# Kernel optimization log

Hardware: AMD Instinct MI355X
Metric: run time of the kernel (lower is better)

## Reference

```python
import jax, jax.numpy as jnp
import numpy as np

EPS_MIN = 1e-8
N_ITER = 50  # solver_iter


def solve_qp_simplex(M, n_iter=N_ITER):
    """Frank-Wolfe min over the simplex of alpha^T M alpha. M: (B,K,K) -> alpha: (B,K)."""
    B, K, _ = M.shape
    alpha0 = jnp.full((B, K), 1.0 / K, dtype=M.dtype)

    def step(alpha, it):
        grad = 2.0 * jnp.einsum('bij,bj->bi', M, alpha)           # (B,K)
        idx = jnp.argmin(grad, axis=1)                             # (B,)
        s = jax.nn.one_hot(idx, K, dtype=alpha.dtype)              # vertex of simplex
        gamma = 2.0 / (it + 2.0)
        return (1.0 - gamma) * alpha + gamma * s, None

    alpha, _ = jax.lax.scan(step, alpha0, jnp.arange(n_iter, dtype=M.dtype))
    return alpha


def _raw_loss(scores, targets, C):
    B, K = scores.shape
    # epsilon = offdiag_mean of C per batch, scaled by 1.0, clamped
    offdiag_mean = (C.sum(axis=(1, 2)) - jnp.trace(C, axis1=1, axis2=2)) / (K * K - K)
    eps = jnp.maximum(offdiag_mean, EPS_MIN)                       # (B,)

    f = 0.5 * scores
    exponent = -(f[:, :, None] + f[:, None, :] + C) / eps[:, None, None]  # (B,K,K)
    shift = exponent.max(axis=(1, 2), keepdims=True)
    logM = exponent - shift
    M = jnp.exp(logM)

    # solver is an implicit layer: non-differentiable by construction
    alpha = jax.lax.stop_gradient(solve_qp_simplex(M, N_ITER))     # (B,K)

    pos = alpha > 0
    loga = jnp.where(pos, jnp.log(jnp.where(pos, alpha, 1.0)), -jnp.inf)
    term = loga[:, :, None] + loga[:, None, :] + logM              # (B,K,K)
    logval = jax.scipy.special.logsumexp(term.reshape(B, K * K), axis=1)
    conjugate = -eps * (logval + shift.reshape(B))

    f_y = jnp.take_along_axis(scores, targets[:, None], axis=1)[:, 0]
    return conjugate - f_y


def setup_inputs() -> dict:
    key = jax.random.key(0)
    k1, k2, k3 = jax.random.split(key, 3)
    B, K = 512, 256
    scores = jax.random.normal(k1, (B, K), dtype=jnp.float32)
    targets = jax.random.randint(k2, (B,), 0, K)
    C = jax.random.uniform(k3, (B, K, K), dtype=jnp.float32)
    return {"scores": scores, "targets": targets, "C": C}


def reference(scores, targets, C):
    return _raw_loss(scores, targets, C).mean()
```

## Files before the change

### kernel.cpp

```cpp
#include <hip/hip_runtime.h>
#include <math.h>

#define KDIM 256
#define NITER 50


__global__ __launch_bounds__(256) void k1_partials(
    const float* __restrict__ scores, const float* __restrict__ C,
    float* __restrict__ psum_o, float* __restrict__ ptrace_o, float* __restrict__ pmin_o)
{
    const int blk = blockIdx.x;
    const int b = blk >> 2, chunk = blk & 3;
    const int tid = threadIdx.x, lane = tid & 63, wave = tid >> 6;
    const float4* C4 = (const float4*)(C + (size_t)b * KDIM * KDIM);

    __shared__ float4 sf4[KDIM/4];
    __shared__ float redS[256], redT[256], redM[256];
    const float* sf = (const float*)sf4;
    ((float*)sf4)[tid] = 0.5f * scores[b*KDIM + tid];
    __syncthreads();

    const int row0 = chunk * 64;
    float psum = 0.f, ptrace = 0.f, pmin = INFINITY;
    #pragma unroll
    for (int rr = 0; rr < 16; ++rr) {
        const int row = row0 + wave + rr*4;
        float4 c4 = C4[row*(KDIM/4) + lane];
        float frow = sf[row];
        float4 fj = sf4[lane];
        psum += (c4.x + c4.y) + (c4.z + c4.w);
        pmin = fminf(pmin, fminf(fminf(frow+fj.x+c4.x, frow+fj.y+c4.y),
                                 fminf(frow+fj.z+c4.z, frow+fj.w+c4.w)));
        if ((row >> 2) == lane) {
            int r2 = row & 3;
            ptrace += (r2==0) ? c4.x : (r2==1) ? c4.y : (r2==2) ? c4.z : c4.w;
        }
    }
    redS[tid] = psum; redT[tid] = ptrace; redM[tid] = pmin;
    __syncthreads();
    for (int s = 128; s > 0; s >>= 1) {
        if (tid < s) {
            redS[tid] += redS[tid+s];
            redT[tid] += redT[tid+s];
            redM[tid]  = fminf(redM[tid], redM[tid+s]);
        }
        __syncthreads();
    }
    if (tid == 0) { psum_o[blk] = redS[0]; ptrace_o[blk] = redT[0]; pmin_o[blk] = redM[0]; }
}

__global__ __launch_bounds__(512) void k23_fw(
    const float* __restrict__ scores, const int* __restrict__ targets,
    const float* __restrict__ C,
    const float* __restrict__ psum_i, const float* __restrict__ ptrace_i, const float* __restrict__ pmin_i,
    float* __restrict__ lossB)
{
    const int b = blockIdx.x;
    const int tid = threadIdx.x, lane = tid & 63, wave = tid >> 6;
    const float* Cb = C + (size_t)b * KDIM * KDIM;
    const float4* C4 = (const float4*)Cb;

    __shared__ float4 sf4[KDIM/4];
    __shared__ float rs[KDIM];
    __shared__ float aAll[KDIM];
    __shared__ int   wcnt[8];
    __shared__ int   sIdx[64];
    __shared__ float sLog[64];
    __shared__ float wm[8], wsm[8];

    const float* sf = (const float*)sf4;
    if (tid < KDIM) ((float*)sf4)[tid] = 0.5f * scores[b*KDIM + tid];
    __syncthreads();

    float sum = 0.f, tr = 0.f, mn = INFINITY;
    #pragma unroll
    for (int c2 = 0; c2 < 4; ++c2) {
        sum += psum_i[b*4 + c2];
        tr  += ptrace_i[b*4 + c2];
        mn   = fminf(mn, pmin_i[b*4 + c2]);
    }
    const float eps = fmaxf((sum - tr) / (float)(KDIM*KDIM - KDIM), 1e-8f);
    const float inv_eps = 1.0f / eps;
    const float minv = mn;

    #pragma unroll 8
    for (int rr = 0; rr < 32; ++rr) {
        const int row = rr*8 + wave;
        float4 c4 = C4[row*(KDIM/4) + lane];
        float frow = sf[row];
        float4 fj = sf4[lane];
        float p = __expf((minv - (frow+fj.x+c4.x)) * inv_eps)
                + __expf((minv - (frow+fj.y+c4.y)) * inv_eps)
                + __expf((minv - (frow+fj.z+c4.z)) * inv_eps)
                + __expf((minv - (frow+fj.w+c4.w)) * inv_eps);
        #pragma unroll
        for (int off = 32; off > 0; off >>= 1) p += __shfl_xor(p, off);
        if (lane == 0) rs[row] = p;
    }
    __syncthreads();

    if (wave == 0) {
        const float f0 = sf[lane], f1 = sf[lane+64], f2 = sf[lane+128], f3 = sf[lane+192];
        const float* r0 = Cb + (size_t)lane*KDIM;
        const float* r1 = r0 + 64*KDIM;
        const float* r2 = r0 + 128*KDIM;
        const float* r3 = r0 + 192*KDIM;

        float v = rs[lane]; int vi = lane;
        float t;
        t = rs[lane+64];  if (t < v) { v = t; vi = lane+64; }
        t = rs[lane+128]; if (t < v) { v = t; vi = lane+128; }
        t = rs[lane+192]; if (t < v) { v = t; vi = lane+192; }
        #pragma unroll
        for (int off = 32; off > 0; off >>= 1) {
            float ov = __shfl_xor(v, off);
            int  ovi = __shfl_xor(vi, off);
            if (ov < v || (ov == v && ovi < vi)) { v = ov; vi = ovi; }
        }
        const int idx0 = vi;

        float fidx = sf[idx0];
        float g0 = 2.0f * __expf((minv - (f0 + fidx + r0[idx0])) * inv_eps);
        float g1 = 2.0f * __expf((minv - (f1 + fidx + r1[idx0])) * inv_eps);
        float g2 = 2.0f * __expf((minv - (f2 + fidx + r2[idx0])) * inv_eps);
        float g3 = 2.0f * __expf((minv - (f3 + fidx + r3[idx0])) * inv_eps);
        float a0 = (lane     == idx0) ? 1.0f : 0.0f;
        float a1 = (lane+64  == idx0) ? 1.0f : 0.0f;
        float a2 = (lane+128 == idx0) ? 1.0f : 0.0f;
        float a3 = (lane+192 == idx0) ? 1.0f : 0.0f;

        for (int it = 1; it < NITER; ++it) {
            float v2 = g0; int vi2 = lane;
            if (g1 < v2) { v2 = g1; vi2 = lane+64; }
            if (g2 < v2) { v2 = g2; vi2 = lane+128; }
            if (g3 < v2) { v2 = g3; vi2 = lane+192; }
            #pragma unroll
            for (int off = 32; off > 0; off >>= 1) {
                float ov = __shfl_xor(v2, off);
                int  ovi = __shfl_xor(vi2, off);
                if (ov < v2 || (ov == v2 && ovi < vi2)) { v2 = ov; vi2 = ovi; }
            }
            const int idx = vi2;
            const float gamma = 2.0f / ((float)it + 2.0f);
            const float omg = 1.0f - gamma;
            const int which = idx >> 6;
            float fsel = (which==0) ? f0 : (which==1) ? f1 : (which==2) ? f2 : f3;
            const float fidx2 = __shfl(fsel, idx & 63);
            const float c0 = r0[idx], c1 = r1[idx], c2_ = r2[idx], c3 = r3[idx];
            g0 = omg*g0 + 2.0f*gamma*__expf((minv - (f0 + fidx2 + c0)) * inv_eps);
            g1 = omg*g1 + 2.0f*gamma*__expf((minv - (f1 + fidx2 + c1)) * inv_eps);
            g2 = omg*g2 + 2.0f*gamma*__expf((minv - (f2 + fidx2 + c2_)) * inv_eps);
            g3 = omg*g3 + 2.0f*gamma*__expf((minv - (f3 + fidx2 + c3)) * inv_eps);
            a0 = omg*a0 + ((lane     == idx) ? gamma : 0.0f);
            a1 = omg*a1 + ((lane+64  == idx) ? gamma : 0.0f);
            a2 = omg*a2 + ((lane+128 == idx) ? gamma : 0.0f);
            a3 = omg*a3 + ((lane+192 == idx) ? gamma : 0.0f);
        }
        aAll[lane]     = a0;
        aAll[lane+64]  = a1;
        aAll[lane+128] = a2;
        aAll[lane+192] = a3;
    }
    __syncthreads();

    const float a = (tid < KDIM) ? aAll[tid] : 0.f;

    unsigned long long mask = __ballot(a > 0.f);
    if (lane == 0) wcnt[wave] = __popcll(mask);
    __syncthreads();
    int off0 = 0;
    for (int w = 0; w < wave; ++w) off0 += wcnt[w];
    int count = 0;
    #pragma unroll
    for (int w = 0; w < 8; ++w) count += wcnt[w];
    if (a > 0.f) {
        int pos = off0 + __popcll(mask & ((1ull << lane) - 1ull));
        sIdx[pos] = tid;
        sLog[pos] = logf(a);
    }
    __syncthreads();

    float m = -INFINITY, ss = 0.f;
    const int total = count * count;
    for (int p = tid; p < total; p += 512) {
        int ii = p / count;
        int jj = p - ii * count;
        int i = sIdx[ii], j = sIdx[jj];
        float cij = Cb[i*KDIM + j];
        float lm = (minv - (sf[i] + sf[j] + cij)) * inv_eps;
        float tt = sLog[ii] + sLog[jj] + lm;
        if (tt > m) { ss = ss * __expf(m - tt) + 1.0f; m = tt; }
        else        { ss += __expf(tt - m); }
    }
    #pragma unroll
    for (int off = 32; off > 0; off >>= 1) {
        float om = __shfl_xor(m, off);
        float os = __shfl_xor(ss, off);
        if (os > 0.f) {
            if (ss <= 0.f)   { m = om; ss = os; }
            else if (om > m) { ss = ss*__expf(m-om) + os; m = om; }
            else             { ss += os*__expf(om-m); }
        }
    }
    if (lane == 0) { wm[wave] = m; wsm[wave] = ss; }
    __syncthreads();
    if (tid == 0) {
        float M = wm[0], S = wsm[0];
        #pragma unroll
        for (int w = 1; w < 8; ++w) {
            float om = wm[w], os = wsm[w];
            if (os > 0.f) {
                if (S <= 0.f)    { M = om; S = os; }
                else if (om > M) { S = S*__expf(M-om) + os; M = om; }
                else             { S += os*__expf(om-M); }
            }
        }
        float logval = M + logf(S);
        float shift = -minv * inv_eps;
        float conjugate = -eps * (logval + shift);
        float fy = scores[b*KDIM + targets[b]];
        lossB[b] = conjugate - fy;
    }
}

__global__ __launch_bounds__(512) void cacis_reduce(const float* __restrict__ lossB,
                                                    float* __restrict__ out, int B)
{
    __shared__ float red[512];
    int t = threadIdx.x;
    red[t] = (t < B) ? lossB[t] : 0.f;
    __syncthreads();
    for (int s = 256; s > 0; s >>= 1) { if (t < s) red[t] += red[t+s]; __syncthreads(); }
    if (t == 0) out[0] = red[0] / (float)B;
}

extern "C" void kernel_launch(void* const* d_in, const int* in_sizes, int n_in,
                              void* d_out, int out_size, void* d_ws, size_t ws_size,
                              hipStream_t stream) {
    const float* scores  = (const float*)d_in[0];
    const int*   targets = (const int*)d_in[1];
    const float* C       = (const float*)d_in[2];
    float* out = (float*)d_out;
    const int B = in_sizes[1];

    float* ws     = (float*)d_ws;
    float* psum   = ws;
    float* ptrace = ws + 2048;
    float* pmin   = ws + 4096;
    float* lossB  = ws + 6144;

    k1_partials<<<B*4, 256, 0, stream>>>(scores, C, psum, ptrace, pmin);
    k23_fw     <<<B,   512, 0, stream>>>(scores, targets, C, psum, ptrace, pmin, lossB);
    cacis_reduce<<<1, 512, 0, stream>>>(lossB, out, B);
}
```

Baseline: 107.9 us.

## Fuse stats and Frank-Wolfe kernels, caching C as fp16 in swizzled LDS

Merges the partial-statistics kernel and the Frank-Wolfe kernel into one 1024-thread block per batch row. Each C matrix is read from global memory once and stored in shared memory as fp16 with an XOR swizzle, so the row-sum, solver and logsumexp stages reuse it from LDS instead of re-reading global memory. This removes a kernel launch and the second full pass over C. In exchange, the 128KB LDS footprint limits occupancy to one block per CU, and C loses precision because it is rounded to half.

```diff
diff --git a/kernel.cpp b/kernel.cpp
--- a/kernel.cpp
+++ b/kernel.cpp
@@ -1,98 +1,89 @@
 #include <hip/hip_runtime.h>
+#include <hip/hip_fp16.h>
 #include <math.h>
 
 #define KDIM 256
 #define NITER 50
 
-
-__global__ __launch_bounds__(256) void k1_partials(
-    const float* __restrict__ scores, const float* __restrict__ C,
-    float* __restrict__ psum_o, float* __restrict__ ptrace_o, float* __restrict__ pmin_o)
+__global__ __launch_bounds__(1024, 1) void cacis_one(
+    const float* __restrict__ scores, const int* __restrict__ targets,
+    const float* __restrict__ C, float* __restrict__ lossB)
 {
-    const int blk = blockIdx.x;
-    const int b = blk >> 2, chunk = blk & 3;
+    const int b = blockIdx.x;
     const int tid = threadIdx.x, lane = tid & 63, wave = tid >> 6;
     const float4* C4 = (const float4*)(C + (size_t)b * KDIM * KDIM);
 
-    __shared__ float4 sf4[KDIM/4];
-    __shared__ float redS[256], redT[256], redM[256];
-    const float* sf = (const float*)sf4;
-    ((float*)sf4)[tid] = 0.5f * scores[b*KDIM + tid];
-    __syncthreads();
-
-    const int row0 = chunk * 64;
+    __shared__ __half Ch[KDIM*KDIM];
+    __shared__ float sf[KDIM];
+    __shared__ float rs[KDIM];
+    __shared__ float aAll[KDIM];
+    __shared__ float wS[16], wT[16], wM[16];
+    __shared__ float bc2[2];
+    __shared__ int   wcnt[16];
+    __shared__ int   sIdx[64];
+    __shared__ float sLog[64];
+    __shared__ float wm[16], wsm[16];
+
+    if (tid < KDIM) sf[tid] = 0.5f * scores[b*KDIM + tid];
+    __syncthreads();
+
+    const int c0 = lane * 4;
+    const float fj0 = sf[c0], fj1 = sf[c0+1], fj2 = sf[c0+2], fj3 = sf[c0+3];
+
     float psum = 0.f, ptrace = 0.f, pmin = INFINITY;
     #pragma unroll
     for (int rr = 0; rr < 16; ++rr) {
-        const int row = row0 + wave + rr*4;
+        const int row = rr*16 + wave;
         float4 c4 = C4[row*(KDIM/4) + lane];
-        float frow = sf[row];
-        float4 fj = sf4[lane];
+        const float frow = sf[row];
         psum += (c4.x + c4.y) + (c4.z + c4.w);
-        pmin = fminf(pmin, fminf(fminf(frow+fj.x+c4.x, frow+fj.y+c4.y),
-                                 fminf(frow+fj.z+c4.z, frow+fj.w+c4.w)));
+        pmin = fminf(pmin, fminf(fminf(frow+fj0+c4.x, frow+fj1+c4.y),
+                                 fminf(frow+fj2+c4.z, frow+fj3+c4.w)));
         if ((row >> 2) == lane) {
             int r2 = row & 3;
             ptrace += (r2==0) ? c4.x : (r2==1) ? c4.y : (r2==2) ? c4.z : c4.w;
         }
-    }
-    redS[tid] = psum; redT[tid] = ptrace; redM[tid] = pmin;
-    __syncthreads();
-    for (int s = 128; s > 0; s >>= 1) {
-        if (tid < s) {
-            redS[tid] += redS[tid+s];
-            redT[tid] += redT[tid+s];
-            redM[tid]  = fminf(redM[tid], redM[tid+s]);
-        }
-        __syncthreads();
-    }
-    if (tid == 0) { psum_o[blk] = redS[0]; ptrace_o[blk] = redT[0]; pmin_o[blk] = redM[0]; }
-}
-
-__global__ __launch_bounds__(512) void k23_fw(
-    const float* __restrict__ scores, const int* __restrict__ targets,
-    const float* __restrict__ C,
-    const float* __restrict__ psum_i, const float* __restrict__ ptrace_i, const float* __restrict__ pmin_i,
-    float* __restrict__ lossB)
-{
-    const int b = blockIdx.x;
-    const int tid = threadIdx.x, lane = tid & 63, wave = tid >> 6;
-    const float* Cb = C + (size_t)b * KDIM * KDIM;
-    const float4* C4 = (const float4*)Cb;
-
-    __shared__ float4 sf4[KDIM/4];
-    __shared__ float rs[KDIM];
-    __shared__ float aAll[KDIM];
-    __shared__ int   wcnt[8];
-    __shared__ int   sIdx[64];
-    __shared__ float sLog[64];
-    __shared__ float wm[8], wsm[8];
-
-    const float* sf = (const float*)sf4;
-    if (tid < KDIM) ((float*)sf4)[tid] = 0.5f * scores[b*KDIM + tid];
-    __syncthreads();
-
-    float sum = 0.f, tr = 0.f, mn = INFINITY;
-    #pragma unroll
-    for (int c2 = 0; c2 < 4; ++c2) {
-        sum += psum_i[b*4 + c2];
-        tr  += ptrace_i[b*4 + c2];
-        mn   = fminf(mn, pmin_i[b*4 + c2]);
-    }
-    const float eps = fmaxf((sum - tr) / (float)(KDIM*KDIM - KDIM), 1e-8f);
+        const int rbase = row * KDIM;
+        const int sw = row & 63;
+        Ch[rbase + ((c0  ) ^ sw)] = __float2half(c4.x);
+        Ch[rbase + ((c0+1) ^ sw)] = __float2half(c4.y);
+        Ch[rbase + ((c0+2) ^ sw)] = __float2half(c4.z);
+        Ch[rbase + ((c0+3) ^ sw)] = __float2half(c4.w);
+    }
+    #pragma unroll
+    for (int off = 32; off > 0; off >>= 1) {
+        psum   += __shfl_xor(psum, off);
+        ptrace += __shfl_xor(ptrace, off);
+        pmin    = fminf(pmin, __shfl_xor(pmin, off));
+    }
+    if (lane == 0) { wS[wave] = psum; wT[wave] = ptrace; wM[wave] = pmin; }
+    __syncthreads();
+    if (tid == 0) {
+        float s = 0.f, t = 0.f, mn = INFINITY;
+        #pragma unroll
+        for (int w = 0; w < 16; ++w) { s += wS[w]; t += wT[w]; mn = fminf(mn, wM[w]); }
+        bc2[0] = mn;
+        bc2[1] = fmaxf((s - t) / (float)(KDIM*KDIM - KDIM), 1e-8f);
+    }
+    __syncthreads();
+    const float minv = bc2[0];
+    const float eps = bc2[1];
     const float inv_eps = 1.0f / eps;
-    const float minv = mn;
-
-    #pragma unroll 8
-    for (int rr = 0; rr < 32; ++rr) {
-        const int row = rr*8 + wave;
-        float4 c4 = C4[row*(KDIM/4) + lane];
-        float frow = sf[row];
-        float4 fj = sf4[lane];
-        float p = __expf((minv - (frow+fj.x+c4.x)) * inv_eps)
-                + __expf((minv - (frow+fj.y+c4.y)) * inv_eps)
-                + __expf((minv - (frow+fj.z+c4.z)) * inv_eps)
-                + __expf((minv - (frow+fj.w+c4.w)) * inv_eps);
+
+    #pragma unroll
+    for (int rr = 0; rr < 16; ++rr) {
+        const int row = rr*16 + wave;
+        const float frow = sf[row];
+        const int rbase = row * KDIM;
+        const int sw = row & 63;
+        const float x0 = __half2float(Ch[rbase + ((c0  ) ^ sw)]);
+        const float x1 = __half2float(Ch[rbase + ((c0+1) ^ sw)]);
+        const float x2 = __half2float(Ch[rbase + ((c0+2) ^ sw)]);
+        const float x3 = __half2float(Ch[rbase + ((c0+3) ^ sw)]);
+        float p = __expf((minv - (frow+fj0+x0)) * inv_eps)
+                + __expf((minv - (frow+fj1+x1)) * inv_eps)
+                + __expf((minv - (frow+fj2+x2)) * inv_eps)
+                + __expf((minv - (frow+fj3+x3)) * inv_eps);
         #pragma unroll
         for (int off = 32; off > 0; off >>= 1) p += __shfl_xor(p, off);
         if (lane == 0) rs[row] = p;
@@ -101,10 +92,7 @@
 
     if (wave == 0) {
         const float f0 = sf[lane], f1 = sf[lane+64], f2 = sf[lane+128], f3 = sf[lane+192];
-        const float* r0 = Cb + (size_t)lane*KDIM;
-        const float* r1 = r0 + 64*KDIM;
-        const float* r2 = r0 + 128*KDIM;
-        const float* r3 = r0 + 192*KDIM;
+        const int base0 = lane*KDIM, base1 = (lane+64)*KDIM, base2 = (lane+128)*KDIM, base3 = (lane+192)*KDIM;
 
         float v = rs[lane]; int vi = lane;
         float t;
@@ -119,11 +107,12 @@
         }
         const int idx0 = vi;
 
-        float fidx = sf[idx0];
-        float g0 = 2.0f * __expf((minv - (f0 + fidx + r0[idx0])) * inv_eps);
-        float g1 = 2.0f * __expf((minv - (f1 + fidx + r1[idx0])) * inv_eps);
-        float g2 = 2.0f * __expf((minv - (f2 + fidx + r2[idx0])) * inv_eps);
-        float g3 = 2.0f * __expf((minv - (f3 + fidx + r3[idx0])) * inv_eps);
+        const float fidx0 = sf[idx0];
+        int sc = idx0 ^ lane;
+        float g0 = 2.0f * __expf((minv - (f0 + fidx0 + __half2float(Ch[base0 + sc]))) * inv_eps);
+        float g1 = 2.0f * __expf((minv - (f1 + fidx0 + __half2float(Ch[base1 + sc]))) * inv_eps);
+        float g2 = 2.0f * __expf((minv - (f2 + fidx0 + __half2float(Ch[base2 + sc]))) * inv_eps);
+        float g3 = 2.0f * __expf((minv - (f3 + fidx0 + __half2float(Ch[base3 + sc]))) * inv_eps);
         float a0 = (lane     == idx0) ? 1.0f : 0.0f;
         float a1 = (lane+64  == idx0) ? 1.0f : 0.0f;
         float a2 = (lane+128 == idx0) ? 1.0f : 0.0f;
@@ -145,12 +134,16 @@
             const float omg = 1.0f - gamma;
             const int which = idx >> 6;
             float fsel = (which==0) ? f0 : (which==1) ? f1 : (which==2) ? f2 : f3;
-            const float fidx2 = __shfl(fsel, idx & 63);
-            const float c0 = r0[idx], c1 = r1[idx], c2_ = r2[idx], c3 = r3[idx];
-            g0 = omg*g0 + 2.0f*gamma*__expf((minv - (f0 + fidx2 + c0)) * inv_eps);
-            g1 = omg*g1 + 2.0f*gamma*__expf((minv - (f1 + fidx2 + c1)) * inv_eps);
-            g2 = omg*g2 + 2.0f*gamma*__expf((minv - (f2 + fidx2 + c2_)) * inv_eps);
-            g3 = omg*g3 + 2.0f*gamma*__expf((minv - (f3 + fidx2 + c3)) * inv_eps);
+            const float fidx = __shfl(fsel, idx & 63);
+            sc = idx ^ lane;
+            const float cc0 = __half2float(Ch[base0 + sc]);
+            const float cc1 = __half2float(Ch[base1 + sc]);
+            const float cc2 = __half2float(Ch[base2 + sc]);
+            const float cc3 = __half2float(Ch[base3 + sc]);
+            g0 = omg*g0 + 2.0f*gamma*__expf((minv - (f0 + fidx + cc0)) * inv_eps);
+            g1 = omg*g1 + 2.0f*gamma*__expf((minv - (f1 + fidx + cc1)) * inv_eps);
+            g2 = omg*g2 + 2.0f*gamma*__expf((minv - (f2 + fidx + cc2)) * inv_eps);
+            g3 = omg*g3 + 2.0f*gamma*__expf((minv - (f3 + fidx + cc3)) * inv_eps);
             a0 = omg*a0 + ((lane     == idx) ? gamma : 0.0f);
             a1 = omg*a1 + ((lane+64  == idx) ? gamma : 0.0f);
             a2 = omg*a2 + ((lane+128 == idx) ? gamma : 0.0f);
@@ -172,7 +165,7 @@
     for (int w = 0; w < wave; ++w) off0 += wcnt[w];
     int count = 0;
     #pragma unroll
-    for (int w = 0; w < 8; ++w) count += wcnt[w];
+    for (int w = 0; w < 16; ++w) count += wcnt[w];
     if (a > 0.f) {
         int pos = off0 + __popcll(mask & ((1ull << lane) - 1ull));
         sIdx[pos] = tid;
@@ -182,11 +175,11 @@
 
     float m = -INFINITY, ss = 0.f;
     const int total = count * count;
-    for (int p = tid; p < total; p += 512) {
+    for (int p = tid; p < total; p += 1024) {
         int ii = p / count;
         int jj = p - ii * count;
         int i = sIdx[ii], j = sIdx[jj];
-        float cij = Cb[i*KDIM + j];
+        float cij = __half2float(Ch[i*KDIM + (j ^ (i & 63))]);
         float lm = (minv - (sf[i] + sf[j] + cij)) * inv_eps;
         float tt = sLog[ii] + sLog[jj] + lm;
         if (tt > m) { ss = ss * __expf(m - tt) + 1.0f; m = tt; }
@@ -207,7 +200,7 @@
     if (tid == 0) {
         float M = wm[0], S = wsm[0];
         #pragma unroll
-        for (int w = 1; w < 8; ++w) {
+        for (int w = 1; w < 16; ++w) {
             float om = wm[w], os = wsm[w];
             if (os > 0.f) {
                 if (S <= 0.f)    { M = om; S = os; }
@@ -243,13 +236,8 @@
     float* out = (float*)d_out;
     const int B = in_sizes[1];
 
-    float* ws     = (float*)d_ws;
-    float* psum   = ws;
-    float* ptrace = ws + 2048;
-    float* pmin   = ws + 4096;
-    float* lossB  = ws + 6144;
-
-    k1_partials<<<B*4, 256, 0, stream>>>(scores, C, psum, ptrace, pmin);
-    k23_fw     <<<B,   512, 0, stream>>>(scores, targets, C, psum, ptrace, pmin, lossB);
+    float* lossB = (float*)d_ws;
+
+    cacis_one  <<<B, 1024, 0, stream>>>(scores, targets, C, lossB);
     cacis_reduce<<<1, 512, 0, stream>>>(lossB, out, B);
 }
```

New measurement: 129.8 us. 20.3% more time.

## Transpose C to fp16 in first pass and split row-sum into separate kernel

Applied to the files above, without the earlier changes.

The first kernel now also writes a transposed half-precision copy of C through an LDS tile. A new kernel computes the exp row sums from that copy with four blocks per batch. The Frank-Wolfe kernel then reads contiguous fp16 columns for its gradient updates instead of strided fp32 elements. This aims to coalesce the serial solver's gathers and spread the exp work across more blocks. In exchange it adds an extra write and read of a 64 MB workspace and an fp16 rounding of C, which can perturb the argmin choices and the final loss.

```diff
diff --git a/kernel.cpp b/kernel.cpp
--- a/kernel.cpp
+++ b/kernel.cpp
@@ -1,41 +1,80 @@
 #include <hip/hip_runtime.h>
+#include <hip/hip_fp16.h>
 #include <math.h>
 
 #define KDIM 256
 #define NITER 50
 
 
-__global__ __launch_bounds__(256) void k1_partials(
+__global__ __launch_bounds__(256, 8) void k1_stream(
     const float* __restrict__ scores, const float* __restrict__ C,
+    __half* __restrict__ CT,
     float* __restrict__ psum_o, float* __restrict__ ptrace_o, float* __restrict__ pmin_o)
 {
     const int blk = blockIdx.x;
     const int b = blk >> 2, chunk = blk & 3;
     const int tid = threadIdx.x, lane = tid & 63, wave = tid >> 6;
     const float4* C4 = (const float4*)(C + (size_t)b * KDIM * KDIM);
-
-    __shared__ float4 sf4[KDIM/4];
+    __half* CTb = CT + (size_t)b * KDIM * KDIM;
+
+    __shared__ float sf[KDIM];
+    __shared__ __half tile[64][34];
     __shared__ float redS[256], redT[256], redM[256];
-    const float* sf = (const float*)sf4;
-    ((float*)sf4)[tid] = 0.5f * scores[b*KDIM + tid];
-    __syncthreads();
-
-    const int row0 = chunk * 64;
+
+    sf[tid] = 0.5f * scores[b*KDIM + tid];
+    __syncthreads();
+
+    const int c0 = lane * 4;
+    const float fj0 = sf[c0], fj1 = sf[c0+1], fj2 = sf[c0+2], fj3 = sf[c0+3];
+    const int jg_own = lane >> 4;
+    const int l16 = lane & 15;
+
     float psum = 0.f, ptrace = 0.f, pmin = INFINITY;
     #pragma unroll
-    for (int rr = 0; rr < 16; ++rr) {
-        const int row = row0 + wave + rr*4;
-        float4 c4 = C4[row*(KDIM/4) + lane];
-        float frow = sf[row];
-        float4 fj = sf4[lane];
-        psum += (c4.x + c4.y) + (c4.z + c4.w);
-        pmin = fminf(pmin, fminf(fminf(frow+fj.x+c4.x, frow+fj.y+c4.y),
-                                 fminf(frow+fj.z+c4.z, frow+fj.w+c4.w)));
-        if ((row >> 2) == lane) {
-            int r2 = row & 3;
-            ptrace += (r2==0) ? c4.x : (r2==1) ? c4.y : (r2==2) ? c4.z : c4.w;
-        }
-    }
+    for (int p = 0; p < 2; ++p) {
+        __half2 st01[8], st23[8];
+        #pragma unroll
+        for (int itL = 0; itL < 8; ++itL) {
+            const int it = p*8 + itL;
+            const int row = chunk*64 + it*4 + wave;
+            float4 c4 = C4[row*(KDIM/4) + lane];
+            const float frow = sf[row];
+            psum += (c4.x + c4.y) + (c4.z + c4.w);
+            pmin = fminf(pmin, fminf(fminf(frow+fj0+c4.x, frow+fj1+c4.y),
+                                     fminf(frow+fj2+c4.z, frow+fj3+c4.w)));
+            if ((row >> 2) == lane) {
+                int r2 = row & 3;
+                ptrace += (r2==0)?c4.x:(r2==1)?c4.y:(r2==2)?c4.z:c4.w;
+            }
+            __half2 h01, h23;
+            h01.x = __float2half_rn(c4.x); h01.y = __float2half_rn(c4.y);
+            h23.x = __float2half_rn(c4.z); h23.y = __float2half_rn(c4.w);
+            st01[itL] = h01; st23[itL] = h23;
+        }
+        #pragma unroll
+        for (int g = 0; g < 4; ++g) {
+            __syncthreads();
+            if (jg_own == g) {
+                const int jl = l16 * 4;
+                #pragma unroll
+                for (int itL = 0; itL < 8; ++itL) {
+                    const int il = itL*4 + wave;
+                    tile[jl+0][il] = st01[itL].x;
+                    tile[jl+1][il] = st01[itL].y;
+                    tile[jl+2][il] = st23[itL].x;
+                    tile[jl+3][il] = st23[itL].y;
+                }
+            }
+            __syncthreads();
+            const int jl = tid >> 2, il0 = (tid & 3) * 8;
+            const uint* src = (const uint*)&tile[jl][il0];
+            uint4 v; v.x = src[0]; v.y = src[1]; v.z = src[2]; v.w = src[3];
+            const int j = g*64 + jl;
+            __half* dst = CTb + j*KDIM + chunk*64 + p*32 + il0;
+            *(uint4*)dst = v;
+        }
+    }
+
     redS[tid] = psum; redT[tid] = ptrace; redM[tid] = pmin;
     __syncthreads();
     for (int s = 128; s > 0; s >>= 1) {
@@ -49,68 +88,108 @@
     if (tid == 0) { psum_o[blk] = redS[0]; ptrace_o[blk] = redT[0]; pmin_o[blk] = redM[0]; }
 }
 
-__global__ __launch_bounds__(512) void k23_fw(
+__global__ __launch_bounds__(256, 8) void k2_rowsums(
+    const float* __restrict__ scores, const __half* __restrict__ CT,
+    const float* __restrict__ psum_i, const float* __restrict__ ptrace_i, const float* __restrict__ pmin_i,
+    float* __restrict__ prs)
+{
+    const int blk = (int)gridDim.x - 1 - (int)blockIdx.x;
+    const int b = blk >> 2, jc = blk & 3;
+    const int tid = threadIdx.x, lane = tid & 63, wave = tid >> 6;
+    const __half* CTb = CT + (size_t)b * KDIM * KDIM;
+
+    __shared__ float sf[KDIM];
+    __shared__ float part[12];
+    __shared__ float bc2[2];
+    __shared__ float racc[4][KDIM];
+
+    sf[tid] = 0.5f * scores[b*KDIM + tid];
+    if (tid < 12) {
+        part[tid] = (tid < 4) ? psum_i[b*4+tid]
+                  : (tid < 8) ? ptrace_i[b*4+tid-4]
+                              : pmin_i[b*4+tid-8];
+    }
+    __syncthreads();
+    if (tid == 0) {
+        float s = part[0]+part[1]+part[2]+part[3];
+        float t = part[4]+part[5]+part[6]+part[7];
+        float mn = fminf(fminf(part[8],part[9]), fminf(part[10],part[11]));
+        bc2[0] = mn;
+        bc2[1] = fmaxf((s - t) / (float)(KDIM*KDIM - KDIM), 1e-8f);
+    }
+    __syncthreads();
+    const float minv = bc2[0];
+    const float inv_eps = 1.0f / bc2[1];
+
+    const int i0 = lane * 4;
+    const float fi0 = sf[i0], fi1 = sf[i0+1], fi2 = sf[i0+2], fi3 = sf[i0+3];
+    float a0 = 0.f, a1 = 0.f, a2 = 0.f, a3 = 0.f;
+    #pragma unroll
+    for (int it = 0; it < 16; ++it) {
+        const int j = jc*64 + it*4 + wave;
+        const __half2* p2 = (const __half2*)(CTb + j*KDIM + i0);
+        __half2 h01 = p2[0], h23 = p2[1];
+        const float base = minv - sf[j];
+        a0 += __expf((base - fi0 - __half2float(h01.x)) * inv_eps);
+        a1 += __expf((base - fi1 - __half2float(h01.y)) * inv_eps);
+        a2 += __expf((base - fi2 - __half2float(h23.x)) * inv_eps);
+        a3 += __expf((base - fi3 - __half2float(h23.y)) * inv_eps);
+    }
+    racc[wave][i0+0] = a0; racc[wave][i0+1] = a1;
+    racc[wave][i0+2] = a2; racc[wave][i0+3] = a3;
+    __syncthreads();
+    prs[(size_t)blk*KDIM + tid] = racc[0][tid]+racc[1][tid]+racc[2][tid]+racc[3][tid];
+}
+
+__global__ __launch_bounds__(256) void k3_fw(
     const float* __restrict__ scores, const int* __restrict__ targets,
-    const float* __restrict__ C,
+    const __half* __restrict__ CT,
     const float* __restrict__ psum_i, const float* __restrict__ ptrace_i, const float* __restrict__ pmin_i,
-    float* __restrict__ lossB)
+    const float* __restrict__ prs, float* __restrict__ lossB)
 {
     const int b = blockIdx.x;
     const int tid = threadIdx.x, lane = tid & 63, wave = tid >> 6;
-    const float* Cb = C + (size_t)b * KDIM * KDIM;
-    const float4* C4 = (const float4*)Cb;
-
-    __shared__ float4 sf4[KDIM/4];
-    __shared__ float rs[KDIM];
+    const __half* CTb = CT + (size_t)b * KDIM * KDIM;
+
+    __shared__ float sf[KDIM];
+    __shared__ float part[12];
+    __shared__ float bc2[2];
+    __shared__ float rsL[KDIM];
     __shared__ float aAll[KDIM];
-    __shared__ int   wcnt[8];
+    __shared__ int   wcnt[4];
     __shared__ int   sIdx[64];
     __shared__ float sLog[64];
-    __shared__ float wm[8], wsm[8];
-
-    const float* sf = (const float*)sf4;
-    if (tid < KDIM) ((float*)sf4)[tid] = 0.5f * scores[b*KDIM + tid];
-    __syncthreads();
-
-    float sum = 0.f, tr = 0.f, mn = INFINITY;
-    #pragma unroll
-    for (int c2 = 0; c2 < 4; ++c2) {
-        sum += psum_i[b*4 + c2];
-        tr  += ptrace_i[b*4 + c2];
-        mn   = fminf(mn, pmin_i[b*4 + c2]);
-    }
-    const float eps = fmaxf((sum - tr) / (float)(KDIM*KDIM - KDIM), 1e-8f);
+    __shared__ float wm[4], wsm[4];
+
+    sf[tid] = 0.5f * scores[b*KDIM + tid];
+    if (tid < 12) {
+        part[tid] = (tid < 4) ? psum_i[b*4+tid]
+                  : (tid < 8) ? ptrace_i[b*4+tid-4]
+                              : pmin_i[b*4+tid-8];
+    }
+    rsL[tid] = prs[(size_t)(b*4+0)*KDIM+tid] + prs[(size_t)(b*4+1)*KDIM+tid]
+             + prs[(size_t)(b*4+2)*KDIM+tid] + prs[(size_t)(b*4+3)*KDIM+tid];
+    __syncthreads();
+    if (tid == 0) {
+        float s = part[0]+part[1]+part[2]+part[3];
+        float t = part[4]+part[5]+part[6]+part[7];
+        float mn = fminf(fminf(part[8],part[9]), fminf(part[10],part[11]));
+        bc2[0] = mn;
+        bc2[1] = fmaxf((s - t) / (float)(KDIM*KDIM - KDIM), 1e-8f);
+    }
+    __syncthreads();
+    const float minv = bc2[0];
+    const float eps = bc2[1];
     const float inv_eps = 1.0f / eps;
-    const float minv = mn;
-
-    #pragma unroll 8
-    for (int rr = 0; rr < 32; ++rr) {
-        const int row = rr*8 + wave;
-        float4 c4 = C4[row*(KDIM/4) + lane];
-        float frow = sf[row];
-        float4 fj = sf4[lane];
-        float p = __expf((minv - (frow+fj.x+c4.x)) * inv_eps)
-                + __expf((minv - (frow+fj.y+c4.y)) * inv_eps)
-                + __expf((minv - (frow+fj.z+c4.z)) * inv_eps)
-                + __expf((minv - (frow+fj.w+c4.w)) * inv_eps);
-        #pragma unroll
-        for (int off = 32; off > 0; off >>= 1) p += __shfl_xor(p, off);
-        if (lane == 0) rs[row] = p;
-    }
-    __syncthreads();
 
     if (wave == 0) {
         const float f0 = sf[lane], f1 = sf[lane+64], f2 = sf[lane+128], f3 = sf[lane+192];
-        const float* r0 = Cb + (size_t)lane*KDIM;
-        const float* r1 = r0 + 64*KDIM;
-        const float* r2 = r0 + 128*KDIM;
-        const float* r3 = r0 + 192*KDIM;
-
-        float v = rs[lane]; int vi = lane;
+
+        float v = rsL[lane]; int vi = lane;
         float t;
-        t = rs[lane+64];  if (t < v) { v = t; vi = lane+64; }
-        t = rs[lane+128]; if (t < v) { v = t; vi = lane+128; }
-        t = rs[lane+192]; if (t < v) { v = t; vi = lane+192; }
+        t = rsL[lane+64];  if (t < v) { v = t; vi = lane+64; }
+        t = rsL[lane+128]; if (t < v) { v = t; vi = lane+128; }
+        t = rsL[lane+192]; if (t < v) { v = t; vi = lane+192; }
         #pragma unroll
         for (int off = 32; off > 0; off >>= 1) {
             float ov = __shfl_xor(v, off);
@@ -119,11 +198,12 @@
         }
         const int idx0 = vi;
 
+        const __half* col0 = CTb + (size_t)idx0 * KDIM;
         float fidx = sf[idx0];
-        float g0 = 2.0f * __expf((minv - (f0 + fidx + r0[idx0])) * inv_eps);
-        float g1 = 2.0f * __expf((minv - (f1 + fidx + r1[idx0])) * inv_eps);
-        float g2 = 2.0f * __expf((minv - (f2 + fidx + r2[idx0])) * inv_eps);
-        float g3 = 2.0f * __expf((minv - (f3 + fidx + r3[idx0])) * inv_eps);
+        float g0 = 2.0f * __expf((minv - (f0 + fidx + __half2float(col0[lane    ]))) * inv_eps);
+        float g1 = 2.0f * __expf((minv - (f1 + fidx + __half2float(col0[lane+64 ]))) * inv_eps);
+        float g2 = 2.0f * __expf((minv - (f2 + fidx + __half2float(col0[lane+128]))) * inv_eps);
+        float g3 = 2.0f * __expf((minv - (f3 + fidx + __half2float(col0[lane+192]))) * inv_eps);
         float a0 = (lane     == idx0) ? 1.0f : 0.0f;
         float a1 = (lane+64  == idx0) ? 1.0f : 0.0f;
         float a2 = (lane+128 == idx0) ? 1.0f : 0.0f;
@@ -146,11 +226,15 @@
             const int which = idx >> 6;
             float fsel = (which==0) ? f0 : (which==1) ? f1 : (which==2) ? f2 : f3;
             const float fidx2 = __shfl(fsel, idx & 63);
-            const float c0 = r0[idx], c1 = r1[idx], c2_ = r2[idx], c3 = r3[idx];
-            g0 = omg*g0 + 2.0f*gamma*__expf((minv - (f0 + fidx2 + c0)) * inv_eps);
-            g1 = omg*g1 + 2.0f*gamma*__expf((minv - (f1 + fidx2 + c1)) * inv_eps);
-            g2 = omg*g2 + 2.0f*gamma*__expf((minv - (f2 + fidx2 + c2_)) * inv_eps);
-            g3 = omg*g3 + 2.0f*gamma*__expf((minv - (f3 + fidx2 + c3)) * inv_eps);
+            const __half* col = CTb + (size_t)idx * KDIM;
+            const float cc0 = __half2float(col[lane    ]);
+            const float cc1 = __half2float(col[lane+64 ]);
+            const float cc2 = __half2float(col[lane+128]);
+            const float cc3 = __half2float(col[lane+192]);
+            g0 = omg*g0 + 2.0f*gamma*__expf((minv - (f0 + fidx2 + cc0)) * inv_eps);
+            g1 = omg*g1 + 2.0f*gamma*__expf((minv - (f1 + fidx2 + cc1)) * inv_eps);
+            g2 = omg*g2 + 2.0f*gamma*__expf((minv - (f2 + fidx2 + cc2)) * inv_eps);
+            g3 = omg*g3 + 2.0f*gamma*__expf((minv - (f3 + fidx2 + cc3)) * inv_eps);
             a0 = omg*a0 + ((lane     == idx) ? gamma : 0.0f);
             a1 = omg*a1 + ((lane+64  == idx) ? gamma : 0.0f);
             a2 = omg*a2 + ((lane+128 == idx) ? gamma : 0.0f);
@@ -163,16 +247,14 @@
     }
     __syncthreads();
 
-    const float a = (tid < KDIM) ? aAll[tid] : 0.f;
+    const float a = aAll[tid];
 
     unsigned long long mask = __ballot(a > 0.f);
     if (lane == 0) wcnt[wave] = __popcll(mask);
     __syncthreads();
     int off0 = 0;
     for (int w = 0; w < wave; ++w) off0 += wcnt[w];
-    int count = 0;
-    #pragma unroll
-    for (int w = 0; w < 8; ++w) count += wcnt[w];
+    const int count = wcnt[0] + wcnt[1] + wcnt[2] + wcnt[3];
     if (a > 0.f) {
         int pos = off0 + __popcll(mask & ((1ull << lane) - 1ull));
         sIdx[pos] = tid;
@@ -182,11 +264,11 @@
 
     float m = -INFINITY, ss = 0.f;
     const int total = count * count;
-    for (int p = tid; p < total; p += 512) {
+    for (int p = tid; p < total; p += KDIM) {
         int ii = p / count;
         int jj = p - ii * count;
         int i = sIdx[ii], j = sIdx[jj];
-        float cij = Cb[i*KDIM + j];
+        float cij = __half2float(CTb[(size_t)j*KDIM + i]);
         float lm = (minv - (sf[i] + sf[j] + cij)) * inv_eps;
         float tt = sLog[ii] + sLog[jj] + lm;
         if (tt > m) { ss = ss * __expf(m - tt) + 1.0f; m = tt; }
@@ -207,7 +289,7 @@
     if (tid == 0) {
         float M = wm[0], S = wsm[0];
         #pragma unroll
-        for (int w = 1; w < 8; ++w) {
+        for (int w = 1; w < 4; ++w) {
             float om = wm[w], os = wsm[w];
             if (os > 0.f) {
                 if (S <= 0.f)    { M = om; S = os; }
@@ -243,13 +325,16 @@
     float* out = (float*)d_out;
     const int B = in_sizes[1];
 
-    float* ws     = (float*)d_ws;
-    float* psum   = ws;
-    float* ptrace = ws + 2048;
-    float* pmin   = ws + 4096;
-    float* lossB  = ws + 6144;
-
-    k1_partials<<<B*4, 256, 0, stream>>>(scores, C, psum, ptrace, pmin);
-    k23_fw     <<<B,   512, 0, stream>>>(scores, targets, C, psum, ptrace, pmin, lossB);
+    __half* CT  = (__half*)d_ws;
+    float* wsf  = (float*)((char*)d_ws + (size_t)67108864);
+    float* psum   = wsf;
+    float* ptrace = wsf + 2048;
+    float* pmin   = wsf + 4096;
+    float* prs    = wsf + 6144;
+    float* lossB  = wsf + 6144 + 524288;
+
+    k1_stream <<<B*4, 256, 0, stream>>>(scores, C, CT, psum, ptrace, pmin);
+    k2_rowsums<<<B*4, 256, 0, stream>>>(scores, CT, psum, ptrace, pmin, prs);
+    k3_fw     <<<B,   256, 0, stream>>>(scores, targets, CT, psum, ptrace, pmin, prs, lossB);
     cacis_reduce<<<1, 512, 0, stream>>>(lossB, out, B);
 }
```

New measurement: 178.7 us. 1.66x slower.

## Fuse three kernels into one cooperative kernel with grid syncs

Applied to the files above, without the earlier changes.

Replaces the three-kernel pipeline with a single cooperative-launch kernel of 1024 blocks (two per batch row). Grid-wide syncs separate the stages: C statistics, then row sums of M written to global, then a one-wave Frank-Wolfe solve driven by per-column gradient updates and a sparse logsumexp over the support of alpha, then the final mean. It aims to remove launch overhead and split the row-sum work across two blocks, at the cost of grid-sync latency and leaving half the blocks idle during the solve. If the cooperative launch fails it falls back to the old kernels.

```diff
diff --git a/kernel.cpp b/kernel.cpp
--- a/kernel.cpp
+++ b/kernel.cpp
@@ -1,9 +1,237 @@
 #include <hip/hip_runtime.h>
+#include <hip/hip_cooperative_groups.h>
 #include <math.h>
 
 #define KDIM 256
 #define NITER 50
 
+namespace cg = cooperative_groups;
+
+
+__global__ __launch_bounds__(256, 4) void cacis_coop(
+    const float* __restrict__ scores, const int* __restrict__ targets,
+    const float* __restrict__ C,
+    float* __restrict__ psum_g, float* __restrict__ ptrace_g, float* __restrict__ pmin_g,
+    float* __restrict__ rs, float* __restrict__ lossB, float* __restrict__ out)
+{
+    cg::grid_group grid = cg::this_grid();
+    const int blk = blockIdx.x;
+    const int b = blk >> 1, half = blk & 1;
+    const int tid = threadIdx.x, lane = tid & 63, wave = tid >> 6;
+    const float* Cb = C + (size_t)b * KDIM * KDIM;
+    const float4* C4 = (const float4*)Cb;
+
+    __shared__ float sf[KDIM];
+    __shared__ float redS[256], redT[256], redM[256];
+    __shared__ float bc2[2];
+    __shared__ float rsL[KDIM];
+    __shared__ float aAll[KDIM];
+    __shared__ int   wcnt[4];
+    __shared__ int   sIdx[64];
+    __shared__ float sLog[64];
+    __shared__ float wm[4], wsm[4];
+
+    sf[tid] = 0.5f * scores[b*KDIM + tid];
+    __syncthreads();
+
+    const int j0 = lane * 4;
+    const float fj0 = sf[j0], fj1 = sf[j0+1], fj2 = sf[j0+2], fj3 = sf[j0+3];
+
+    const int row0 = half * 128;
+    float psum = 0.f, ptrace = 0.f, pmin = INFINITY;
+    #pragma unroll 8
+    for (int rr = 0; rr < 32; ++rr) {
+        const int row = row0 + wave + rr*4;
+        float4 c4 = C4[row*(KDIM/4) + lane];
+        const float frow = sf[row];
+        psum += (c4.x + c4.y) + (c4.z + c4.w);
+        pmin = fminf(pmin, fminf(fminf(frow+fj0+c4.x, frow+fj1+c4.y),
+                                 fminf(frow+fj2+c4.z, frow+fj3+c4.w)));
+        if ((row >> 2) == lane) {
+            int r2 = row & 3;
+            ptrace += (r2==0)?c4.x:(r2==1)?c4.y:(r2==2)?c4.z:c4.w;
+        }
+    }
+    redS[tid] = psum; redT[tid] = ptrace; redM[tid] = pmin;
+    __syncthreads();
+    for (int s = 128; s > 0; s >>= 1) {
+        if (tid < s) {
+            redS[tid] += redS[tid+s];
+            redT[tid] += redT[tid+s];
+            redM[tid]  = fminf(redM[tid], redM[tid+s]);
+        }
+        __syncthreads();
+    }
+    if (tid == 0) { psum_g[blk] = redS[0]; ptrace_g[blk] = redT[0]; pmin_g[blk] = redM[0]; }
+
+    grid.sync();
+
+    if (tid == 0) {
+        float s  = psum_g[b*2]   + psum_g[b*2+1];
+        float t  = ptrace_g[b*2] + ptrace_g[b*2+1];
+        float mn = fminf(pmin_g[b*2], pmin_g[b*2+1]);
+        bc2[0] = mn;
+        bc2[1] = fmaxf((s - t) / (float)(KDIM*KDIM - KDIM), 1e-8f);
+    }
+    __syncthreads();
+    const float minv = bc2[0];
+    const float eps = bc2[1];
+    const float inv_eps = 1.0f / eps;
+
+    #pragma unroll 4
+    for (int r = 0; r < 32; ++r) {
+        const int row = row0 + wave*32 + r;
+        float4 c4 = C4[row*(KDIM/4) + lane];
+        const float base = minv - sf[row];
+        float p = __expf((base - fj0 - c4.x) * inv_eps)
+                + __expf((base - fj1 - c4.y) * inv_eps)
+                + __expf((base - fj2 - c4.z) * inv_eps)
+                + __expf((base - fj3 - c4.w) * inv_eps);
+        #pragma unroll
+        for (int off = 32; off > 0; off >>= 1) p += __shfl_xor(p, off);
+        if (lane == 0) rs[b*KDIM + row] = p;
+    }
+
+    grid.sync();
+
+    if (half == 0) {
+        rsL[tid] = rs[b*KDIM + tid];
+        __syncthreads();
+
+        if (wave == 0) {
+            const float f0 = sf[lane], f1 = sf[lane+64], f2 = sf[lane+128], f3 = sf[lane+192];
+            const float* r0 = Cb + (size_t)lane*KDIM;
+            const float* r1 = r0 + 64*KDIM;
+            const float* r2 = r0 + 128*KDIM;
+            const float* r3 = r0 + 192*KDIM;
+
+            float v = rsL[lane]; int vi = lane;
+            float t;
+            t = rsL[lane+64];  if (t < v) { v = t; vi = lane+64; }
+            t = rsL[lane+128]; if (t < v) { v = t; vi = lane+128; }
+            t = rsL[lane+192]; if (t < v) { v = t; vi = lane+192; }
+            #pragma unroll
+            for (int off = 32; off > 0; off >>= 1) {
+                float ov = __shfl_xor(v, off);
+                int  ovi = __shfl_xor(vi, off);
+                if (ov < v || (ov == v && ovi < vi)) { v = ov; vi = ovi; }
+            }
+            const int idx0 = vi;
+
+            float fidx = sf[idx0];
+            float g0 = 2.0f * __expf((minv - (f0 + fidx + r0[idx0])) * inv_eps);
+            float g1 = 2.0f * __expf((minv - (f1 + fidx + r1[idx0])) * inv_eps);
+            float g2 = 2.0f * __expf((minv - (f2 + fidx + r2[idx0])) * inv_eps);
+            float g3 = 2.0f * __expf((minv - (f3 + fidx + r3[idx0])) * inv_eps);
+            float a0 = (lane     == idx0) ? 1.0f : 0.0f;
+            float a1 = (lane+64  == idx0) ? 1.0f : 0.0f;
+            float a2 = (lane+128 == idx0) ? 1.0f : 0.0f;
+            float a3 = (lane+192 == idx0) ? 1.0f : 0.0f;
+
+            for (int it = 1; it < NITER; ++it) {
+                float v2 = g0; int vi2 = lane;
+                if (g1 < v2) { v2 = g1; vi2 = lane+64; }
+                if (g2 < v2) { v2 = g2; vi2 = lane+128; }
+                if (g3 < v2) { v2 = g3; vi2 = lane+192; }
+                #pragma unroll
+                for (int off = 32; off > 0; off >>= 1) {
+                    float ov = __shfl_xor(v2, off);
+                    int  ovi = __shfl_xor(vi2, off);
+                    if (ov < v2 || (ov == v2 && ovi < vi2)) { v2 = ov; vi2 = ovi; }
+                }
+                const int idx = vi2;
+                const float gamma = 2.0f / ((float)it + 2.0f);
+                const float omg = 1.0f - gamma;
+                const int which = idx >> 6;
+                float fsel = (which==0) ? f0 : (which==1) ? f1 : (which==2) ? f2 : f3;
+                const float fidx2 = __shfl(fsel, idx & 63);
+                const float cc0 = r0[idx], cc1 = r1[idx], cc2 = r2[idx], cc3 = r3[idx];
+                g0 = omg*g0 + 2.0f*gamma*__expf((minv - (f0 + fidx2 + cc0)) * inv_eps);
+                g1 = omg*g1 + 2.0f*gamma*__expf((minv - (f1 + fidx2 + cc1)) * inv_eps);
+                g2 = omg*g2 + 2.0f*gamma*__expf((minv - (f2 + fidx2 + cc2)) * inv_eps);
+                g3 = omg*g3 + 2.0f*gamma*__expf((minv - (f3 + fidx2 + cc3)) * inv_eps);
+                a0 = omg*a0 + ((lane     == idx) ? gamma : 0.0f);
+                a1 = omg*a1 + ((lane+64  == idx) ? gamma : 0.0f);
+                a2 = omg*a2 + ((lane+128 == idx) ? gamma : 0.0f);
+                a3 = omg*a3 + ((lane+192 == idx) ? gamma : 0.0f);
+            }
+            aAll[lane]     = a0;
+            aAll[lane+64]  = a1;
+            aAll[lane+128] = a2;
+            aAll[lane+192] = a3;
+        }
+        __syncthreads();
+
+        const float a = aAll[tid];
+
+        unsigned long long mask = __ballot(a > 0.f);
+        if (lane == 0) wcnt[wave] = __popcll(mask);
+        __syncthreads();
+        int off0 = 0;
+        for (int w = 0; w < wave; ++w) off0 += wcnt[w];
+        const int count = wcnt[0] + wcnt[1] + wcnt[2] + wcnt[3];
+        if (a > 0.f) {
+            int pos = off0 + __popcll(mask & ((1ull << lane) - 1ull));
+            sIdx[pos] = tid;
+            sLog[pos] = logf(a);
+        }
+        __syncthreads();
+
+        float m = -INFINITY, ss = 0.f;
+        const int total = count * count;
+        for (int p = tid; p < total; p += KDIM) {
+            int ii = p / count;
+            int jj = p - ii * count;
+            int i = sIdx[ii], j = sIdx[jj];
+            float cij = Cb[i*KDIM + j];
+            float lm = (minv - (sf[i] + sf[j] + cij)) * inv_eps;
+            float tt = sLog[ii] + sLog[jj] + lm;
+            if (tt > m) { ss = ss * __expf(m - tt) + 1.0f; m = tt; }
+            else        { ss += __expf(tt - m); }
+        }
+        #pragma unroll
+        for (int off = 32; off > 0; off >>= 1) {
+            float om = __shfl_xor(m, off);
+            float os = __shfl_xor(ss, off);
+            if (os > 0.f) {
+                if (ss <= 0.f)   { m = om; ss = os; }
+                else if (om > m) { ss = ss*__expf(m-om) + os; m = om; }
+                else             { ss += os*__expf(om-m); }
+            }
+        }
+        if (lane == 0) { wm[wave] = m; wsm[wave] = ss; }
+        __syncthreads();
+        if (tid == 0) {
+            float M = wm[0], S = wsm[0];
+            #pragma unroll
+            for (int w = 1; w < 4; ++w) {
+                float om = wm[w], os = wsm[w];
+                if (os > 0.f) {
+                    if (S <= 0.f)    { M = om; S = os; }
+                    else if (om > M) { S = S*__expf(M-om) + os; M = om; }
+                    else             { S += os*__expf(om-M); }
+                }
+            }
+            float logval = M + logf(S);
+            float shift = -minv * inv_eps;
+            float conjugate = -eps * (logval + shift);
+            float fy = scores[b*KDIM + targets[b]];
+            lossB[b] = conjugate - fy;
+        }
+    }
+
+    grid.sync();
+
+    if (blk == 0) {
+        redS[tid] = lossB[tid] + lossB[tid + 256];
+        __syncthreads();
+        for (int s = 128; s > 0; s >>= 1) {
+            if (tid < s) redS[tid] += redS[tid+s];
+            __syncthreads();
+        }
+        if (tid == 0) out[0] = redS[0] / 512.0f;
+    }
+}
 
 __global__ __launch_bounds__(256) void k1_partials(
     const float* __restrict__ scores, const float* __restrict__ C,
@@ -247,7 +475,18 @@
     float* psum   = ws;
     float* ptrace = ws + 2048;
     float* pmin   = ws + 4096;
-    float* lossB  = ws + 6144;
+    float* rs     = ws + 6144;
+    float* lossB  = ws + 6144 + 131072;
+
+    void* args[] = {
+        (void*)&scores, (void*)&targets, (void*)&C,
+        (void*)&psum, (void*)&ptrace, (void*)&pmin,
+        (void*)&rs, (void*)&lossB, (void*)&out
+    };
+    hipError_t err = hipLaunchCooperativeKernel((const void*)cacis_coop,
+                                                dim3(1024), dim3(256),
+                                                args, 0, stream);
+    if (err == hipSuccess) return;
 
     k1_partials<<<B*4, 256, 0, stream>>>(scores, C, psum, ptrace, pmin);
     k23_fw     <<<B,   512, 0, stream>>>(scores, targets, C, psum, ptrace, pmin, lossB);
```

New measurement: 407.6 us. 278% more time.
